# Performance work log

Measured on AMD Instinct MI355X. Metric: run time of the kernel, lower is better.

## Reference

```python
import jax, jax.numpy as jnp
import numpy as np

D_MODEL = 512
NUM_HEADS = 8
HEAD_DIM = D_MODEL // NUM_HEADS
CTX = 20
EPS = 1e-5


def _layernorm(x, w, b):
    mu = jnp.mean(x, axis=-1, keepdims=True)
    var = jnp.var(x, axis=-1, keepdims=True)
    return (x - mu) * jax.lax.rsqrt(var + EPS) * w + b


def setup_inputs() -> dict:
    key = jax.random.key(0)
    ks = jax.random.split(key, 12)
    B, T = 4096, CTX
    s_attn = 1.0 / np.sqrt(D_MODEL)
    s_ffn1 = 1.0 / np.sqrt(D_MODEL)
    s_ffn2 = 1.0 / np.sqrt(4 * D_MODEL)
    return {
        "x": jax.random.normal(ks[0], (B, T, D_MODEL), dtype=jnp.float32),
        "ln1_w": jnp.ones((D_MODEL,), jnp.float32),
        "ln1_b": jnp.zeros((D_MODEL,), jnp.float32),
        # per-head projections stacked: [H, D, head_dim]
        "Wq": jax.random.normal(ks[1], (NUM_HEADS, D_MODEL, HEAD_DIM), dtype=jnp.float32) * s_attn,
        "Wk": jax.random.normal(ks[2], (NUM_HEADS, D_MODEL, HEAD_DIM), dtype=jnp.float32) * s_attn,
        "Wv": jax.random.normal(ks[3], (NUM_HEADS, D_MODEL, HEAD_DIM), dtype=jnp.float32) * s_attn,
        "Wo": jax.random.normal(ks[4], (D_MODEL, D_MODEL), dtype=jnp.float32) * s_attn,
        "Wo_b": jnp.zeros((D_MODEL,), jnp.float32),
        "ln2_w": jnp.ones((D_MODEL,), jnp.float32),
        "ln2_b": jnp.zeros((D_MODEL,), jnp.float32),
        "W1": jax.random.normal(ks[5], (D_MODEL, 4 * D_MODEL), dtype=jnp.float32) * s_ffn1,
        "b1": jnp.zeros((4 * D_MODEL,), jnp.float32),
        "W2": jax.random.normal(ks[6], (4 * D_MODEL, D_MODEL), dtype=jnp.float32) * s_ffn2,
        "b2": jnp.zeros((D_MODEL,), jnp.float32),
    }


def reference(x, ln1_w, ln1_b, Wq, Wk, Wv, Wo, Wo_b, ln2_w, ln2_b, W1, b1, W2, b2):
    B, T, D = x.shape
    # --- multi-head attention (dropout = identity, eval mode) ---
    h = _layernorm(x, ln1_w, ln1_b)
    # [B,T,D] x [H,D,hd] -> [B,H,T,hd]
    q = jnp.einsum('btd,hde->bhte', h, Wq)
    k = jnp.einsum('btd,hde->bhte', h, Wk)
    v = jnp.einsum('btd,hde->bhte', h, Wv)
    scores = jnp.einsum('bhte,bhse->bhts', q, k) / np.sqrt(HEAD_DIM)
    mask = jnp.tril(jnp.ones((T, T), dtype=bool))
    scores = jnp.where(mask, scores, -jnp.inf)
    attn = jax.nn.softmax(scores, axis=-1)
    ctx = jnp.einsum('bhts,bhse->bhte', attn, v)  # [B,H,T,hd]
    # concat heads along last dim (head order matches torch cat)
    ctx = jnp.transpose(ctx, (0, 2, 1, 3)).reshape(B, T, D)
    attn_out = ctx @ Wo.T + Wo_b
    x = x + attn_out
    # --- FFN ---
    h2 = _layernorm(x, ln2_w, ln2_b)
    ff = jax.nn.relu(h2 @ W1 + b1) @ W2 + b2
    return x + ff
```

## Files before the change

kernel.cpp:

```cpp
#include <hip/hip_runtime.h>

typedef __attribute__((ext_vector_type(8))) short short8;
typedef __attribute__((ext_vector_type(4))) float float4v;

__device__ __forceinline__ float b2f(ushort u) {
  union { uint i; float f; } c; c.i = ((uint)u) << 16; return c.f;
}
__device__ __forceinline__ ushort f2b(float f) {
  union { float f; uint i; } c; c.f = f;
  return (ushort)((c.i + 0x7fffu + ((c.i >> 16) & 1u)) >> 16);
}
__device__ __forceinline__ float ldin(const void* p, size_t i, int f32) {
  return f32 ? ((const float*)p)[i] : b2f(((const ushort*)p)[i]);
}
__device__ __forceinline__ void load_lds16(const ushort* g, ushort* l) {
  __builtin_amdgcn_global_load_lds((__attribute__((address_space(1))) const void*)g,
                                   (__attribute__((address_space(3))) void*)l, 16, 0, 0);
}

__global__ void detect(const void* w1, int* flag) {
  const uint u = *(const uint*)w1;
  *flag = (u == 0x3F800000u) ? 1 : 0;
}

__global__ __launch_bounds__(256) void gemm_bt(
    const ushort* __restrict__ A, const ushort* __restrict__ B,
    void* C, const ushort* __restrict__ bias, const void* res,
    const int* resflagp, const int* outflagp,
    int M, int N, int K, int relu, int nb)
{
  __shared__ ushort lA[128 * 64];
  __shared__ ushort lB[128 * 64];
  const int w = threadIdx.x >> 6;
  const int l = threadIdx.x & 63;
  const int bid = blockIdx.x;
  const int low3 = bid & 7, rest = bid >> 3;
  const int n_idx = rest % nb;
  const int band  = ((rest / nb) << 3) | low3;
  const int mBase = band * 128;
  const int nBase = n_idx * 128;
  const int wr = w >> 1, wc = w & 1;
  const int lrow = l >> 3;
  const int lcolsw = (((l & 7) ^ lrow) * 8);

  const float4v vzero = {0.f, 0.f, 0.f, 0.f};
  float4v acc[4][4];
#pragma unroll
  for (int i = 0; i < 4; ++i)
#pragma unroll
    for (int j = 0; j < 4; ++j) acc[i][j] = vzero;

  for (int k0 = 0; k0 < K; k0 += 64) {
#pragma unroll
    for (int i = 0; i < 4; ++i) {
      const int s = w + i * 4;
      load_lds16(A + (size_t)(mBase + s * 8 + lrow) * K + k0 + lcolsw, &lA[s * 512]);
      load_lds16(B + (size_t)(nBase + s * 8 + lrow) * K + k0 + lcolsw, &lB[s * 512]);
    }
    __syncthreads();
#pragma unroll
    for (int kk = 0; kk < 64; kk += 32) {
      const int ch = (kk >> 3) + (l >> 4);
      const int csw = (ch ^ (l & 7)) * 8;
      short8 af[4], bf[4];
#pragma unroll
      for (int i = 0; i < 4; ++i)
        af[i] = *(const short8*)&lA[(wr * 64 + i * 16 + (l & 15)) * 64 + csw];
#pragma unroll
      for (int j = 0; j < 4; ++j)
        bf[j] = *(const short8*)&lB[(wc * 64 + j * 16 + (l & 15)) * 64 + csw];
#pragma unroll
      for (int i = 0; i < 4; ++i)
#pragma unroll
        for (int j = 0; j < 4; ++j)
          acc[i][j] = __builtin_amdgcn_mfma_f32_16x16x32_bf16(af[i], bf[j], acc[i][j], 0, 0, 0);
    }
    __syncthreads();
  }

  const int rf32 = (res && resflagp) ? *resflagp : 0;
  const int of32 = outflagp ? *outflagp : 0;
  const int r0 = mBase + wr * 64 + (l >> 4) * 4;
  const int c0 = nBase + wc * 64 + (l & 15);
#pragma unroll
  for (int j = 0; j < 4; ++j) {
    const int col = c0 + j * 16;
    const float bv = bias ? b2f(bias[col]) : 0.f;
#pragma unroll
    for (int i = 0; i < 4; ++i) {
#pragma unroll
      for (int r = 0; r < 4; ++r) {
        const size_t off = (size_t)(r0 + i * 16 + r) * N + col;
        float v = acc[i][j][r] + bv;
        if (res) v += rf32 ? ((const float*)res)[off] : b2f(((const ushort*)res)[off]);
        if (relu) v = fmaxf(v, 0.f);
        if (of32) ((float*)C)[off] = v;
        else      ((ushort*)C)[off] = f2b(v);
      }
    }
  }
}

__global__ __launch_bounds__(256) void lnorm(const void* __restrict__ x,
                                             const ushort* __restrict__ gw,
                                             const ushort* __restrict__ gb,
                                             ushort* __restrict__ out,
                                             ushort* __restrict__ xcopy,
                                             const int* flagp)
{
  const int f32 = flagp ? *flagp : 0;
  const int tok = blockIdx.x * 4 + (threadIdx.x >> 6);
  const int l = threadIdx.x & 63;
  const size_t base = (size_t)tok * 512 + l * 8;
  float v[8];
  if (f32) {
    const float4* p = (const float4*)((const float*)x + base);
    float4 a = p[0], b = p[1];
    v[0]=a.x; v[1]=a.y; v[2]=a.z; v[3]=a.w; v[4]=b.x; v[5]=b.y; v[6]=b.z; v[7]=b.w;
  } else {
    uint4 u = *(const uint4*)((const ushort*)x + base);
    uint uu[4] = {u.x, u.y, u.z, u.w};
#pragma unroll
    for (int i = 0; i < 4; ++i) {
      v[2*i]   = b2f((ushort)(uu[i] & 0xffffu));
      v[2*i+1] = b2f((ushort)(uu[i] >> 16));
    }
  }
  if (xcopy) {
    uint xo[4];
#pragma unroll
    for (int i = 0; i < 4; ++i)
      xo[i] = (uint)f2b(v[2*i]) | ((uint)f2b(v[2*i+1]) << 16);
    uint4 xv; xv.x = xo[0]; xv.y = xo[1]; xv.z = xo[2]; xv.w = xo[3];
    *(uint4*)(xcopy + base) = xv;
  }
  float s = 0.f, ss = 0.f;
#pragma unroll
  for (int i = 0; i < 8; ++i) { s += v[i]; ss += v[i] * v[i]; }
  for (int off = 32; off > 0; off >>= 1) {
    s  += __shfl_xor(s, off, 64);
    ss += __shfl_xor(ss, off, 64);
  }
  const float mean = s * (1.f / 512.f);
  const float var  = ss * (1.f / 512.f) - mean * mean;
  const float inv  = rsqrtf(var + 1e-5f);
  uint4 uwv = *(const uint4*)(gw + l * 8);
  uint4 ubv = *(const uint4*)(gb + l * 8);
  uint uws[4] = {uwv.x, uwv.y, uwv.z, uwv.w};
  uint ubs[4] = {ubv.x, ubv.y, ubv.z, ubv.w};
  uint ro[4];
#pragma unroll
  for (int i = 0; i < 4; ++i) {
    float w0 = b2f((ushort)(uws[i] & 0xffffu)), w1 = b2f((ushort)(uws[i] >> 16));
    float b0 = b2f((ushort)(ubs[i] & 0xffffu)), b1 = b2f((ushort)(ubs[i] >> 16));
    float y0 = (v[2*i]   - mean) * inv * w0 + b0;
    float y1 = (v[2*i+1] - mean) * inv * w1 + b1;
    ro[i] = (uint)f2b(y0) | ((uint)f2b(y1) << 16);
  }
  uint4 o; o.x = ro[0]; o.y = ro[1]; o.z = ro[2]; o.w = ro[3];
  *(uint4*)(out + base) = o;
}

__global__ __launch_bounds__(128) void attn(const ushort* __restrict__ QKV,
                                            ushort* __restrict__ ctx)
{
  __shared__ float sq[2][20][65];
  __shared__ float sk[2][20][65];
  __shared__ float sv[2][20][65];
  __shared__ float sp[2][20][33];
  const int w = threadIdx.x >> 6;
  const int l = threadIdx.x & 63;
  const int idx = blockIdx.x * 2 + w;
  const int b = idx >> 3, h = idx & 7;
  const ushort* base = QKV + (size_t)b * 20 * 1536 + h * 64;
#pragma unroll
  for (int tp = 0; tp < 10; ++tp) {
    const int t = tp * 2 + (l >> 5);
    const int e2 = (l & 31) * 2;
    const uint uq = *(const uint*)&base[t * 1536 + e2];
    const uint uk = *(const uint*)&base[t * 1536 + 512 + e2];
    const uint uv = *(const uint*)&base[t * 1536 + 1024 + e2];
    sq[w][t][e2] = b2f((ushort)(uq & 0xffffu)); sq[w][t][e2+1] = b2f((ushort)(uq >> 16));
    sk[w][t][e2] = b2f((ushort)(uk & 0xffffu)); sk[w][t][e2+1] = b2f((ushort)(uk >> 16));
    sv[w][t][e2] = b2f((ushort)(uv & 0xffffu)); sv[w][t][e2+1] = b2f((ushort)(uv >> 16));
  }
  __syncthreads();
  for (int tp = 0; tp < 10; ++tp) {
    const int t = tp * 2 + (l >> 5);
    const int s = l & 31;
    const int sr = (s < 20) ? s : 19;
    float d = 0.f;
#pragma unroll 8
    for (int e = 0; e < 64; ++e) d += sq[w][t][e] * sk[w][sr][e];
    const bool valid = (s <= t) && (s < 20);
    float sc = valid ? d * 0.125f : -1e30f;
    float m = sc;
    for (int off = 16; off > 0; off >>= 1) m = fmaxf(m, __shfl_xor(m, off, 32));
    float p = valid ? __expf(sc - m) : 0.f;
    float sum = p;
    for (int off = 16; off > 0; off >>= 1) sum += __shfl_xor(sum, off, 32);
    if (s < 20) sp[w][t][s] = p / sum;
  }
  __syncthreads();
  ushort* cbase = ctx + (size_t)b * 20 * 512 + h * 64 + l;
  for (int t = 0; t < 20; ++t) {
    float o = 0.f;
    for (int s = 0; s <= t; ++s) o += sp[w][t][s] * sv[w][s][l];
    cbase[t * 512] = f2b(o);
  }
}

__global__ __launch_bounds__(256) void pack_w(
    const void* Wq, const void* Wk, const void* Wv, const void* Wo,
    const void* W1, const void* W2,
    const void* ln1w, const void* ln1b, const void* ln2w, const void* ln2b,
    const void* Wob, const void* b1v, const void* b2v,
    const int* flagp,
    ushort* __restrict__ Wqkv_t, ushort* __restrict__ W1_t,
    ushort* __restrict__ W2_t, ushort* __restrict__ Wo_c,
    ushort* __restrict__ smalls)
{
  const int f32 = *flagp;
  const int i = blockIdx.x * 256 + threadIdx.x;
  if (i < 786432) {
    const int m = i / 262144;
    const int r = i - m * 262144;
    const void* src = (m == 0) ? Wq : ((m == 1) ? Wk : Wv);
    const int hh = r >> 15, d = (r >> 6) & 511, e = r & 63;
    Wqkv_t[(size_t)(m * 512 + hh * 64 + e) * 512 + d] = f2b(ldin(src, r, f32));
  } else if (i < 1835008) {
    const int r = i - 786432;
    const int d = r >> 11, f = r & 2047;
    W1_t[(size_t)f * 512 + d] = f2b(ldin(W1, r, f32));
  } else if (i < 2883584) {
    const int r = i - 1835008;
    const int f = r >> 9, o = r & 511;
    W2_t[(size_t)o * 2048 + f] = f2b(ldin(W2, r, f32));
  } else if (i < 3145728) {
    const int r = i - 2883584;
    Wo_c[r] = f2b(ldin(Wo, r, f32));
  } else {
    const int r = i - 3145728;
    const void* src; int idx;
    if      (r < 512)  { src = ln1w; idx = r; }
    else if (r < 1024) { src = ln1b; idx = r - 512; }
    else if (r < 1536) { src = ln2w; idx = r - 1024; }
    else if (r < 2048) { src = ln2b; idx = r - 1536; }
    else if (r < 2560) { src = Wob;  idx = r - 2048; }
    else if (r < 3072) { src = b2v;  idx = r - 2560; }
    else               { src = b1v;  idx = r - 3072; }
    smalls[r] = f2b(ldin(src, idx, f32));
  }
}

extern "C" void kernel_launch(void* const* d_in, const int* in_sizes, int n_in,
                              void* d_out, int out_size, void* d_ws, size_t ws_size,
                              hipStream_t stream) {
  char* ws = (char*)d_ws;
  int*    flag   = (int*)ws;
  ushort* Wqkv_t = (ushort*)(ws + 4096);
  ushort* W1_t   = (ushort*)(ws + 1576960ull);
  ushort* W2_t   = (ushort*)(ws + 3674112ull);
  ushort* Wo_c   = (ushort*)(ws + 5771264ull);
  ushort* smalls = (ushort*)(ws + 6295552ull);
  ushort* QKV    = (ushort*)(ws + 8388608ull);
  ushort* ff1    = QKV;
  ushort* ctxb   = (ushort*)(ws + 260046848ull);
  ushort* h      = (ushort*)(ws + 343932928ull);
  ushort* x2     = (ushort*)(ws + 427819008ull);
  ushort* xbf    = (ushort*)(ws + 511705088ull);
  const bool have_xbf = ws_size >= 595591168ull;

  detect<<<1, 1, 0, stream>>>(d_in[1], flag);
  pack_w<<<12308, 256, 0, stream>>>(d_in[3], d_in[4], d_in[5], d_in[6],
                                    d_in[10], d_in[12],
                                    d_in[1], d_in[2], d_in[8], d_in[9],
                                    d_in[7], d_in[11], d_in[13],
                                    flag, Wqkv_t, W1_t, W2_t, Wo_c, smalls);
  lnorm<<<20480, 256, 0, stream>>>(d_in[0], smalls + 0, smalls + 512, h,
                                   have_xbf ? xbf : nullptr, flag);
  gemm_bt<<<12 * 640, 256, 0, stream>>>(h, Wqkv_t, QKV, nullptr, nullptr,
                                        nullptr, nullptr, 81920, 1536, 512, 0, 12);
  attn<<<16384, 128, 0, stream>>>(QKV, ctxb);
  gemm_bt<<<4 * 640, 256, 0, stream>>>(ctxb, Wo_c, x2, smalls + 2048,
                                       have_xbf ? (const void*)xbf : (const void*)d_in[0],
                                       have_xbf ? nullptr : flag, nullptr,
                                       81920, 512, 512, 0, 4);
  lnorm<<<20480, 256, 0, stream>>>(x2, smalls + 1024, smalls + 1536, h, nullptr, nullptr);
  gemm_bt<<<16 * 640, 256, 0, stream>>>(h, W1_t, ff1, smalls + 3072, nullptr,
                                        nullptr, nullptr, 81920, 2048, 512, 1, 16);
  gemm_bt<<<4 * 640, 256, 0, stream>>>(ff1, W2_t, d_out, smalls + 2560, x2,
                                       nullptr, flag, 81920, 512, 2048, 0, 4);
}
```

Before: 1.687 ms.

## Replace 128x128 GEMM with 256x256 double-buffered pipelined GEMM kernel

Replaces the 128x128-tile, 4-wave GEMM with a 256x256-tile, 8-wave kernel. It double-buffers the A and B LDS tiles and interleaves global-to-LDS loads for the next k-step with MFMA work on the current one, using explicit waitcnt, sched barriers and setprio. The larger tiles raise operand reuse and cut global traffic, and the prefetch schedule hides load latency. The cost is 128KB of LDS per block and many accumulators, which limits occupancy, and the hand-written vmcnt counts must match the issued loads exactly or the results will be wrong.

New measurement: 1.971 ms. +16.9%, slower.

```diff
diff --git a/kernel.cpp b/kernel.cpp
--- a/kernel.cpp
+++ b/kernel.cpp
@@ -17,81 +17,139 @@
   __builtin_amdgcn_global_load_lds((__attribute__((address_space(1))) const void*)g,
                                    (__attribute__((address_space(3))) void*)l, 16, 0, 0);
 }
+__device__ __forceinline__ void wg_barrier() {
+  asm volatile("" ::: "memory");
+  __builtin_amdgcn_s_barrier();
+  asm volatile("" ::: "memory");
+}
 
 __global__ void detect(const void* w1, int* flag) {
   const uint u = *(const uint*)w1;
   *flag = (u == 0x3F800000u) ? 1 : 0;
 }
 
-__global__ __launch_bounds__(256) void gemm_bt(
+__global__ __launch_bounds__(512, 2) void gemm256(
     const ushort* __restrict__ A, const ushort* __restrict__ B,
     void* C, const ushort* __restrict__ bias, const void* res,
     const int* resflagp, const int* outflagp,
     int M, int N, int K, int relu, int nb)
 {
-  __shared__ ushort lA[128 * 64];
-  __shared__ ushort lB[128 * 64];
-  const int w = threadIdx.x >> 6;
-  const int l = threadIdx.x & 63;
+  __shared__ ushort lA[2][256 * 64];
+  __shared__ ushort lB[2][256 * 64];
+  const int tid = threadIdx.x;
+  const int w = tid >> 6, l = tid & 63;
+  const int wr = w >> 2, wc = w & 3;
   const int bid = blockIdx.x;
   const int low3 = bid & 7, rest = bid >> 3;
   const int n_idx = rest % nb;
   const int band  = ((rest / nb) << 3) | low3;
-  const int mBase = band * 128;
-  const int nBase = n_idx * 128;
-  const int wr = w >> 1, wc = w & 1;
+  const int mBase = band * 256;
+  const int nBase = n_idx * 256;
   const int lrow = l >> 3;
   const int lcolsw = (((l & 7) ^ lrow) * 8);
-
-  const float4v vzero = {0.f, 0.f, 0.f, 0.f};
-  float4v acc[4][4];
-#pragma unroll
-  for (int i = 0; i < 4; ++i)
-#pragma unroll
-    for (int j = 0; j < 4; ++j) acc[i][j] = vzero;
-
-  for (int k0 = 0; k0 < K; k0 += 64) {
-#pragma unroll
-    for (int i = 0; i < 4; ++i) {
-      const int s = w + i * 4;
-      load_lds16(A + (size_t)(mBase + s * 8 + lrow) * K + k0 + lcolsw, &lA[s * 512]);
-      load_lds16(B + (size_t)(nBase + s * 8 + lrow) * K + k0 + lcolsw, &lB[s * 512]);
-    }
-    __syncthreads();
-#pragma unroll
-    for (int kk = 0; kk < 64; kk += 32) {
-      const int ch = (kk >> 3) + (l >> 4);
-      const int csw = (ch ^ (l & 7)) * 8;
-      short8 af[4], bf[4];
-#pragma unroll
-      for (int i = 0; i < 4; ++i)
-        af[i] = *(const short8*)&lA[(wr * 64 + i * 16 + (l & 15)) * 64 + csw];
-#pragma unroll
-      for (int j = 0; j < 4; ++j)
-        bf[j] = *(const short8*)&lB[(wc * 64 + j * 16 + (l & 15)) * 64 + csw];
-#pragma unroll
-      for (int i = 0; i < 4; ++i)
-#pragma unroll
-        for (int j = 0; j < 4; ++j)
-          acc[i][j] = __builtin_amdgcn_mfma_f32_16x16x32_bf16(af[i], bf[j], acc[i][j], 0, 0, 0);
-    }
-    __syncthreads();
-  }
+  const int cs0 = (((l >> 4) + 0) ^ (l & 7)) << 3;
+  const int cs1 = (((l >> 4) + 4) ^ (l & 7)) << 3;
+  const int arow0 = wr * 128 + (l & 15);
+  const int brow0 = wc * 64 + (l & 15);
+  const int NT = K >> 6;
+
+  auto STAGE = [&](const ushort* __restrict__ Gp, int rb, ushort* ldsOp, int segBase, int kof) {
+#pragma unroll
+    for (int j = 0; j < 2; ++j) {
+      const int s = segBase + j * 8 + w;
+      load_lds16(Gp + (size_t)(rb + s * 8 + lrow) * K + kof + lcolsw, ldsOp + s * 512);
+    }
+  };
+
+  const float4v vz = {0.f, 0.f, 0.f, 0.f};
+  float4v acc[8][4];
+#pragma unroll
+  for (int i = 0; i < 8; ++i)
+#pragma unroll
+    for (int j = 0; j < 4; ++j) acc[i][j] = vz;
+
+  STAGE(A, mBase, &lA[0][0], 0, 0);  STAGE(A, mBase, &lA[0][0], 16, 0);
+  STAGE(B, nBase, &lB[0][0], 0, 0);  STAGE(B, nBase, &lB[0][0], 16, 0);
+  const int kp1 = (NT > 1 ? 64 : 0);
+  STAGE(B, nBase, &lB[1][0], 0, kp1); STAGE(B, nBase, &lB[1][0], 16, kp1);
+
+  short8 bf[4][2], af[2][2];
+
+  for (int t = 0; t < NT; ++t) {
+    const int cur = t & 1;
+    ushort* lAc = &lA[cur][0];
+    ushort* lAn = &lA[cur ^ 1][0];
+    ushort* lBc = &lB[cur][0];
+    const int kA1 = (t + 1 < NT ? t + 1 : NT - 1) << 6;
+    const int kB2 = (t + 2 < NT ? t + 2 : NT - 1) << 6;
+
+    STAGE(A, mBase, lAn, 0, kA1);
+    asm volatile("s_waitcnt vmcnt(6)" ::: "memory");
+    __builtin_amdgcn_sched_barrier(0);
+    wg_barrier();
+#pragma unroll
+    for (int nj = 0; nj < 4; ++nj) {
+      bf[nj][0] = *(const short8*)&lBc[(brow0 + nj * 16) * 64 + cs0];
+      bf[nj][1] = *(const short8*)&lBc[(brow0 + nj * 16) * 64 + cs1];
+    }
+    af[0][0] = *(const short8*)&lAc[(arow0 + 0) * 64 + cs0];
+    af[0][1] = *(const short8*)&lAc[(arow0 + 0) * 64 + cs1];
+    af[1][0] = *(const short8*)&lAc[(arow0 + 16) * 64 + cs0];
+    af[1][1] = *(const short8*)&lAc[(arow0 + 16) * 64 + cs1];
+    asm volatile("s_waitcnt lgkmcnt(0)" ::: "memory");
+    __builtin_amdgcn_sched_barrier(0);
+    __builtin_amdgcn_s_setprio(1);
+#pragma unroll
+    for (int i = 0; i < 2; ++i)
+#pragma unroll
+      for (int nj = 0; nj < 4; ++nj) {
+        acc[i][nj] = __builtin_amdgcn_mfma_f32_16x16x32_bf16(af[i][0], bf[nj][0], acc[i][nj], 0, 0, 0);
+        acc[i][nj] = __builtin_amdgcn_mfma_f32_16x16x32_bf16(af[i][1], bf[nj][1], acc[i][nj], 0, 0, 0);
+      }
+    __builtin_amdgcn_s_setprio(0);
+    wg_barrier();
+
+#pragma unroll
+    for (int p = 1; p < 4; ++p) {
+      if (p == 1)      STAGE(A, mBase, lAn, 16, kA1);
+      else if (p == 2) STAGE(B, nBase, lBc, 0, kB2);
+      else             STAGE(B, nBase, lBc, 16, kB2);
+      af[0][0] = *(const short8*)&lAc[(arow0 + (2 * p) * 16) * 64 + cs0];
+      af[0][1] = *(const short8*)&lAc[(arow0 + (2 * p) * 16) * 64 + cs1];
+      af[1][0] = *(const short8*)&lAc[(arow0 + (2 * p + 1) * 16) * 64 + cs0];
+      af[1][1] = *(const short8*)&lAc[(arow0 + (2 * p + 1) * 16) * 64 + cs1];
+      wg_barrier();
+      asm volatile("s_waitcnt lgkmcnt(0)" ::: "memory");
+      __builtin_amdgcn_sched_barrier(0);
+      __builtin_amdgcn_s_setprio(1);
+#pragma unroll
+      for (int i = 0; i < 2; ++i)
+#pragma unroll
+        for (int nj = 0; nj < 4; ++nj) {
+          acc[2 * p + i][nj] = __builtin_amdgcn_mfma_f32_16x16x32_bf16(af[i][0], bf[nj][0], acc[2 * p + i][nj], 0, 0, 0);
+          acc[2 * p + i][nj] = __builtin_amdgcn_mfma_f32_16x16x32_bf16(af[i][1], bf[nj][1], acc[2 * p + i][nj], 0, 0, 0);
+        }
+      __builtin_amdgcn_s_setprio(0);
+      wg_barrier();
+    }
+  }
+  asm volatile("s_waitcnt vmcnt(0)" ::: "memory");
+  __builtin_amdgcn_sched_barrier(0);
 
   const int rf32 = (res && resflagp) ? *resflagp : 0;
   const int of32 = outflagp ? *outflagp : 0;
-  const int r0 = mBase + wr * 64 + (l >> 4) * 4;
+  const int r0 = mBase + wr * 128 + (l >> 4) * 4;
   const int c0 = nBase + wc * 64 + (l & 15);
 #pragma unroll
-  for (int j = 0; j < 4; ++j) {
-    const int col = c0 + j * 16;
+  for (int nj = 0; nj < 4; ++nj) {
+    const int col = c0 + nj * 16;
     const float bv = bias ? b2f(bias[col]) : 0.f;
 #pragma unroll
-    for (int i = 0; i < 4; ++i) {
-#pragma unroll
-      for (int r = 0; r < 4; ++r) {
-        const size_t off = (size_t)(r0 + i * 16 + r) * N + col;
-        float v = acc[i][j][r] + bv;
+    for (int mi = 0; mi < 8; ++mi) {
+#pragma unroll
+      for (int rr = 0; rr < 4; ++rr) {
+        const size_t off = (size_t)(r0 + mi * 16 + rr) * N + col;
+        float v = acc[mi][nj][rr] + bv;
         if (res) v += rf32 ? ((const float*)res)[off] : b2f(((const ushort*)res)[off]);
         if (relu) v = fmaxf(v, 0.f);
         if (of32) ((float*)C)[off] = v;
@@ -279,16 +337,16 @@
                                     flag, Wqkv_t, W1_t, W2_t, Wo_c, smalls);
   lnorm<<<20480, 256, 0, stream>>>(d_in[0], smalls + 0, smalls + 512, h,
                                    have_xbf ? xbf : nullptr, flag);
-  gemm_bt<<<12 * 640, 256, 0, stream>>>(h, Wqkv_t, QKV, nullptr, nullptr,
-                                        nullptr, nullptr, 81920, 1536, 512, 0, 12);
+  gemm256<<<6 * 320, 512, 0, stream>>>(h, Wqkv_t, QKV, nullptr, nullptr,
+                                       nullptr, nullptr, 81920, 1536, 512, 0, 6);
   attn<<<16384, 128, 0, stream>>>(QKV, ctxb);
-  gemm_bt<<<4 * 640, 256, 0, stream>>>(ctxb, Wo_c, x2, smalls + 2048,
+  gemm256<<<2 * 320, 512, 0, stream>>>(ctxb, Wo_c, x2, smalls + 2048,
                                        have_xbf ? (const void*)xbf : (const void*)d_in[0],
                                        have_xbf ? nullptr : flag, nullptr,
-                                       81920, 512, 512, 0, 4);
+                                       81920, 512, 512, 0, 2);
   lnorm<<<20480, 256, 0, stream>>>(x2, smalls + 1024, smalls + 1536, h, nullptr, nullptr);
-  gemm_bt<<<16 * 640, 256, 0, stream>>>(h, W1_t, ff1, smalls + 3072, nullptr,
-                                        nullptr, nullptr, 81920, 2048, 512, 1, 16);
-  gemm_bt<<<4 * 640, 256, 0, stream>>>(ff1, W2_t, d_out, smalls + 2560, x2,
-                                       nullptr, flag, 81920, 512, 2048, 0, 4);
-}
+  gemm256<<<8 * 320, 512, 0, stream>>>(h, W1_t, ff1, smalls + 3072, nullptr,
+                                       nullptr, nullptr, 81920, 2048, 512, 1, 8);
+  gemm256<<<2 * 320, 512, 0, stream>>>(ff1, W2_t, d_out, smalls + 2560, x2,
+                                       nullptr, flag, 81920, 512, 2048, 0, 2);
+}
```

## Double-buffer A tile and software-pipeline GEMM main loop with explicit waitcnts

Applied to the files above, without the earlier changes.

The GEMM main loop now double-buffers the A tile in LDS and issues the next A tile's global-to-LDS load before computing the current one. B is single-buffered and reloaded after the trailing barrier. LDS reads use inline ds_read_b128 with explicit lgkmcnt waits so the first half of the MFMAs can start while the second half's fragments are still arriving, and MFMA sections run at raised wave priority. Launch bounds request 3 blocks per CU. The aim is to hide global load latency and LDS read latency behind matrix math, at the cost of more LDS, possible register pressure, and fragile hand-written wait counts.

Result: faster. 1.572 ms (-6.8%).

```diff
diff --git a/kernel.cpp b/kernel.cpp
--- a/kernel.cpp
+++ b/kernel.cpp
@@ -17,19 +17,30 @@
   __builtin_amdgcn_global_load_lds((__attribute__((address_space(1))) const void*)g,
                                    (__attribute__((address_space(3))) void*)l, 16, 0, 0);
 }
+typedef __attribute__((address_space(3))) const ushort* lds_cp;
+__device__ __forceinline__ short8 ldsr128(const ushort* p) {
+  short8 r;
+  asm volatile("ds_read_b128 %0, %1" : "=v"(r) : "v"((lds_cp)p));
+  return r;
+}
+__device__ __forceinline__ void wg_barrier() {
+  asm volatile("" ::: "memory");
+  __builtin_amdgcn_s_barrier();
+  asm volatile("" ::: "memory");
+}
 
 __global__ void detect(const void* w1, int* flag) {
   const uint u = *(const uint*)w1;
   *flag = (u == 0x3F800000u) ? 1 : 0;
 }
 
-__global__ __launch_bounds__(256) void gemm_bt(
+__global__ __launch_bounds__(256, 3) void gemm_bt(
     const ushort* __restrict__ A, const ushort* __restrict__ B,
     void* C, const ushort* __restrict__ bias, const void* res,
     const int* resflagp, const int* outflagp,
     int M, int N, int K, int relu, int nb)
 {
-  __shared__ ushort lA[128 * 64];
+  __shared__ ushort lA[2][128 * 64];
   __shared__ ushort lB[128 * 64];
   const int w = threadIdx.x >> 6;
   const int l = threadIdx.x & 63;
@@ -42,6 +53,24 @@
   const int wr = w >> 1, wc = w & 1;
   const int lrow = l >> 3;
   const int lcolsw = (((l & 7) ^ lrow) * 8);
+  const int cs0 = (((l >> 4) + 0) ^ (l & 7)) << 3;
+  const int cs1 = (((l >> 4) + 4) ^ (l & 7)) << 3;
+  const int NT = K >> 6;
+
+  auto STAGE_A = [&](ushort* dst, int kof) {
+#pragma unroll
+    for (int i = 0; i < 4; ++i) {
+      const int s = w + i * 4;
+      load_lds16(A + (size_t)(mBase + s * 8 + lrow) * K + kof + lcolsw, dst + s * 512);
+    }
+  };
+  auto STAGE_B = [&](int kof) {
+#pragma unroll
+    for (int i = 0; i < 4; ++i) {
+      const int s = w + i * 4;
+      load_lds16(B + (size_t)(nBase + s * 8 + lrow) * K + kof + lcolsw, &lB[s * 512]);
+    }
+  };
 
   const float4v vzero = {0.f, 0.f, 0.f, 0.f};
   float4v acc[4][4];
@@ -50,33 +79,49 @@
 #pragma unroll
     for (int j = 0; j < 4; ++j) acc[i][j] = vzero;
 
-  for (int k0 = 0; k0 < K; k0 += 64) {
-#pragma unroll
-    for (int i = 0; i < 4; ++i) {
-      const int s = w + i * 4;
-      load_lds16(A + (size_t)(mBase + s * 8 + lrow) * K + k0 + lcolsw, &lA[s * 512]);
-      load_lds16(B + (size_t)(nBase + s * 8 + lrow) * K + k0 + lcolsw, &lB[s * 512]);
-    }
-    __syncthreads();
-#pragma unroll
-    for (int kk = 0; kk < 64; kk += 32) {
-      const int ch = (kk >> 3) + (l >> 4);
-      const int csw = (ch ^ (l & 7)) * 8;
-      short8 af[4], bf[4];
-#pragma unroll
-      for (int i = 0; i < 4; ++i)
-        af[i] = *(const short8*)&lA[(wr * 64 + i * 16 + (l & 15)) * 64 + csw];
+  STAGE_A(&lA[0][0], 0);
+  STAGE_B(0);
+
+  for (int t = 0; t < NT; ++t) {
+    const int kn = (t + 1 < NT ? t + 1 : NT - 1) << 6;
+    STAGE_A(&lA[(t + 1) & 1][0], kn);
+    asm volatile("s_waitcnt vmcnt(4)" ::: "memory");
+    __builtin_amdgcn_sched_barrier(0);
+    wg_barrier();
+
+    const ushort* lAc = &lA[t & 1][0];
+    short8 a0[4], b0[4], a1[4], b1[4];
+#pragma unroll
+    for (int i = 0; i < 4; ++i) a0[i] = ldsr128(&lAc[(wr * 64 + i * 16 + (l & 15)) * 64 + cs0]);
+#pragma unroll
+    for (int j = 0; j < 4; ++j) b0[j] = ldsr128(&lB[(wc * 64 + j * 16 + (l & 15)) * 64 + cs0]);
+#pragma unroll
+    for (int i = 0; i < 4; ++i) a1[i] = ldsr128(&lAc[(wr * 64 + i * 16 + (l & 15)) * 64 + cs1]);
+#pragma unroll
+    for (int j = 0; j < 4; ++j) b1[j] = ldsr128(&lB[(wc * 64 + j * 16 + (l & 15)) * 64 + cs1]);
+    asm volatile("s_waitcnt lgkmcnt(8)" ::: "memory");
+    __builtin_amdgcn_sched_barrier(0);
+    __builtin_amdgcn_s_setprio(1);
+#pragma unroll
+    for (int i = 0; i < 4; ++i)
 #pragma unroll
       for (int j = 0; j < 4; ++j)
-        bf[j] = *(const short8*)&lB[(wc * 64 + j * 16 + (l & 15)) * 64 + csw];
-#pragma unroll
-      for (int i = 0; i < 4; ++i)
-#pragma unroll
-        for (int j = 0; j < 4; ++j)
-          acc[i][j] = __builtin_amdgcn_mfma_f32_16x16x32_bf16(af[i], bf[j], acc[i][j], 0, 0, 0);
-    }
-    __syncthreads();
-  }
+        acc[i][j] = __builtin_amdgcn_mfma_f32_16x16x32_bf16(a0[i], b0[j], acc[i][j], 0, 0, 0);
+    __builtin_amdgcn_s_setprio(0);
+    asm volatile("s_waitcnt lgkmcnt(0)" ::: "memory");
+    __builtin_amdgcn_sched_barrier(0);
+    __builtin_amdgcn_s_setprio(1);
+#pragma unroll
+    for (int i = 0; i < 4; ++i)
+#pragma unroll
+      for (int j = 0; j < 4; ++j)
+        acc[i][j] = __builtin_amdgcn_mfma_f32_16x16x32_bf16(a1[i], b1[j], acc[i][j], 0, 0, 0);
+    __builtin_amdgcn_s_setprio(0);
+    wg_barrier();
+    STAGE_B(kn);
+  }
+  asm volatile("s_waitcnt vmcnt(0)" ::: "memory");
+  __builtin_amdgcn_sched_barrier(0);
 
   const int rf32 = (res && resflagp) ? *resflagp : 0;
   const int of32 = outflagp ? *outflagp : 0;
```
